# Performance work log

Hardware: AMD Instinct MI355X
Metric: run time of the kernel (lower is better)

## Reference

```python
import jax, jax.numpy as jnp
import numpy as np

B, T, C, H = 2, 2048, 1024, 16
D = C // H  # head_dim = 64

def setup_inputs() -> dict:
    key = jax.random.key(0)
    ks = jax.random.split(key, 5)
    x = jax.random.normal(ks[0], (B, T, C), dtype=jnp.float32)
    Wqkv = jax.random.normal(ks[1], (C, 3 * C), dtype=jnp.float32) * 0.02
    bqkv = jnp.zeros((3 * C,), dtype=jnp.float32)
    Wout = jax.random.normal(ks[2], (C, C), dtype=jnp.float32) * 0.02
    bout = jnp.zeros((C,), dtype=jnp.float32)
    return {"x": x, "Wqkv": Wqkv, "bqkv": bqkv, "Wout": Wout, "bout": bout}

def reference(x, Wqkv, bqkv, Wout, bout):
    Bb, Tt, Cc = x.shape
    qkv = x @ Wqkv + bqkv                       # [B,T,3C]
    qkv = qkv.reshape(Bb, Tt, 3, H, D)
    qkv = jnp.transpose(qkv, (2, 0, 3, 1, 4))   # [3,B,H,T,D]
    q, k, v = qkv[0], qkv[1], qkv[2]
    scale = 1.0 / np.sqrt(D).astype(np.float32)
    scores = jnp.einsum('bhqd,bhkd->bhqk', q, k) * scale  # [B,H,T,T]
    causal = jnp.tril(jnp.ones((Tt, Tt), dtype=bool))
    scores = jnp.where(causal[None, None, :, :], scores, jnp.float32(-jnp.inf))
    attn = jax.nn.softmax(scores, axis=-1)
    out = jnp.einsum('bhqk,bhkd->bhqd', attn, v)          # [B,H,T,D]
    out = jnp.transpose(out, (0, 2, 1, 3)).reshape(Bb, Tt, Cc)
    return out @ Wout + bout
```

## Files before the change

### kernel.cpp

```cpp
#include <hip/hip_runtime.h>

#define Bc 2
#define Tc 2048
#define Cc 1024
#define Hc 16
#define Dc 64
#define Mtot (Bc*Tc)
#define Kdim Cc
#define N1 (3*Cc)
#define N2 Cc

typedef __attribute__((ext_vector_type(8))) short short8;
typedef __attribute__((ext_vector_type(4))) float float4v;
typedef __attribute__((ext_vector_type(2))) unsigned int uint2v;
typedef __attribute__((ext_vector_type(4))) unsigned int uint4v;

#define HAVE_PLSWAP (__has_builtin(__builtin_amdgcn_permlane32_swap) && __has_builtin(__builtin_amdgcn_permlane16_swap))

__device__ __forceinline__ unsigned short f2bf(float f) {
  unsigned int u = __builtin_bit_cast(unsigned int, f);
  u += 0x7FFFu + ((u >> 16) & 1u);
  return (unsigned short)(u >> 16);
}

__device__ __forceinline__ unsigned int pk_bf16(float a, float b) {
#if __has_builtin(__builtin_amdgcn_cvt_pk_bf16_f32)
  typedef __attribute__((ext_vector_type(2))) __bf16 bf16x2;
  bf16x2 v = __builtin_amdgcn_cvt_pk_bf16_f32(a, b);
  return __builtin_bit_cast(unsigned int, v);
#else
  return (unsigned int)f2bf(a) | ((unsigned int)f2bf(b) << 16);
#endif
}

__device__ __forceinline__ float fast_exp2(float x) {
#if __has_builtin(__builtin_amdgcn_exp2f)
  return __builtin_amdgcn_exp2f(x);
#else
  return exp2f(x);
#endif
}

__device__ __forceinline__ void gl2lds16(const unsigned short* g, unsigned short* l) {
  __builtin_amdgcn_global_load_lds((const __attribute__((address_space(1))) void*)g,
                                   (__attribute__((address_space(3))) void*)l, 16, 0, 0);
}

#if HAVE_PLSWAP
__device__ __forceinline__ short8 pv_frag(unsigned int a, unsigned int b,
                                          unsigned int c, unsigned int d) {
  uint2v r0 = __builtin_amdgcn_permlane32_swap(a, c, false, false);
  uint2v r1 = __builtin_amdgcn_permlane16_swap(r0[0], r0[1], false, false);
  uint2v r2 = __builtin_amdgcn_permlane32_swap(b, d, false, false);
  uint2v r3 = __builtin_amdgcn_permlane16_swap(r2[0], r2[1], false, false);
  uint4v w = {r1[0], r3[0], r1[1], r3[1]};
  return __builtin_bit_cast(short8, w);
}
#endif

__global__ __launch_bounds__(256) void k_prep(const float* __restrict__ wqkv,
                                              const float* __restrict__ wout,
                                              const float* __restrict__ x,
                                              unsigned short* __restrict__ wqkvT,
                                              unsigned short* __restrict__ woutT,
                                              unsigned short* __restrict__ xb) {
  const int bx = blockIdx.x;
  if (bx >= 128) {
    int idx = ((bx - 128) * 32 + blockIdx.y) * 256 + threadIdx.x;
    float4 v = ((const float4*)x)[idx];
    uint2 o;
    o.x = pk_bf16(v.x, v.y);
    o.y = pk_bf16(v.z, v.w);
    ((uint2*)xb)[idx] = o;
    return;
  }
  __shared__ float tile[32][33];
  const float* w;  unsigned short* wT;  int N, n0;
  if (bx < 96) { w = wqkv; wT = wqkvT; N = N1; n0 = bx * 32; }
  else         { w = wout; wT = woutT; N = N2; n0 = (bx - 96) * 32; }
  const int k0 = blockIdx.y * 32;
  int tx = threadIdx.x & 31, ty = threadIdx.x >> 5;
  for (int i = 0; i < 4; ++i)
    tile[ty + 8*i][tx] = w[(size_t)(k0 + ty + 8*i) * N + n0 + tx];
  __syncthreads();
  for (int i = 0; i < 4; ++i)
    wT[(size_t)(n0 + ty + 8*i) * Kdim + k0 + tx] = f2bf(tile[tx][ty + 8*i]);
}

#define STAGE64(Abase, Bbase, dst, kb)                                          \
  for (int h2 = 0; h2 < 2; ++h2) {                                              \
    unsigned short* sa = (dst) + h2*4096;                                       \
    unsigned short* sb = (dst) + 8192 + h2*4096;                                \
    gl2lds16((Abase) + (size_t)(m0+row0)*Kdim + (kb) + 32*h2 + ko0, sa + c0*8); \
    gl2lds16((Abase) + (size_t)(m0+row1)*Kdim + (kb) + 32*h2 + ko1, sa + c1*8); \
    gl2lds16((Bbase) + (size_t)(n0+row0)*Kdim + (kb) + 32*h2 + ko0, sb + c0*8); \
    gl2lds16((Bbase) + (size_t)(n0+row1)*Kdim + (kb) + 32*h2 + ko1, sb + c1*8); \
  }

__global__ __launch_bounds__(256) void k_gemm_qkv(const unsigned short* __restrict__ A,
                                                  const unsigned short* __restrict__ BT,
                                                  const float* __restrict__ bias,
                                                  unsigned short* __restrict__ qkv) {
  __shared__ alignas(16) unsigned short smem[32768];
  const int m0 = blockIdx.y * 128, n0 = blockIdx.x * 128;
  const int tid = threadIdx.x;
  const int w = tid >> 6, lane = tid & 63;
  const int ln = lane & 15, qd = lane >> 4;
  const int wm = w >> 1, wn = w & 1;
  const int c0 = tid, c1 = tid + 256;
  const int row0 = c0 >> 2, ko0 = (c0 & 3) * 8;
  const int row1 = c1 >> 2, ko1 = (c1 & 3) * 8;
  const float4v zero4 = {0.f, 0.f, 0.f, 0.f};
  float4v acc[4][4];
  for (int i = 0; i < 4; ++i) for (int j = 0; j < 4; ++j) acc[i][j] = zero4;

  STAGE64(A, BT, smem, 0);
  int cur = 0;
  for (int kk = 0; kk < Kdim; kk += 64) {
    __syncthreads();
    if (kk + 64 < Kdim) {
      unsigned short* nb = smem + (cur ^ 1) * 16384;
      STAGE64(A, BT, nb, kk + 64);
    }
    const unsigned short* buf = smem + cur * 16384;
    for (int h = 0; h < 2; ++h) {
      const unsigned short* As = buf + h*4096;
      const unsigned short* Bs = buf + 8192 + h*4096;
      short8 af[4], bf[4];
      for (int i = 0; i < 4; ++i)
        af[i] = *(const short8*)(As + (wm*64 + i*16 + ln) * 32 + qd*8);
      for (int j = 0; j < 4; ++j)
        bf[j] = *(const short8*)(Bs + (wn*64 + j*16 + ln) * 32 + qd*8);
      for (int i = 0; i < 4; ++i)
        for (int j = 0; j < 4; ++j)
          acc[i][j] = __builtin_amdgcn_mfma_f32_16x16x32_bf16(af[i], bf[j], acc[i][j], 0, 0, 0);
    }
    cur ^= 1;
  }
  const int s = n0 >> 10;
  if (s < 2) {
    const float scale = (s == 0) ? 0.18033688f : 1.0f;
    for (int i = 0; i < 4; ++i) {
      int mbase = m0 + wm*64 + i*16 + qd*4;
      for (int j = 0; j < 4; ++j) {
        int ncol = n0 + wn*64 + j*16 + ln;
        float bv = bias[ncol];
        int rem = ncol & 1023;
        int h = rem >> 6, d = rem & 63;
        for (int r = 0; r < 4; ++r) {
          int m = mbase + r;
          int b = m >> 11, t = m & 2047;
          float val = (acc[i][j][r] + bv) * scale;
          qkv[((((size_t)s*Bc + b)*Hc + h)*Tc + t)*Dc + d] = f2bf(val);
        }
      }
    }
  } else {
    unsigned short* vbase = qkv + (size_t)2*Bc*Hc*Tc*Dc;
    const int b = m0 >> 11, t0 = m0 & 2047;
    const int h0 = (n0 & 1023) >> 6;
    for (int p = 0; p < 2; ++p) {
      __syncthreads();
      if (wn == p) {
        for (int i = 0; i < 4; ++i) {
          int tl = wm*64 + i*16 + qd*4;
          for (int j = 0; j < 4; ++j) {
            int dl = j*16 + ln;
            float bv = bias[n0 + p*64 + dl];
            uint2 pk;
            pk.x = pk_bf16(acc[i][j][0] + bv, acc[i][j][1] + bv);
            pk.y = pk_bf16(acc[i][j][2] + bv, acc[i][j][3] + bv);
            *(uint2*)(smem + dl*136 + tl) = pk;
          }
        }
      }
      __syncthreads();
      for (int ii = 0; ii < 4; ++ii) {
        int idx = tid + 256*ii;
        int row = idx >> 4, c16 = idx & 15;
        int4 v = *(const int4*)(smem + row*136 + c16*8);
        *(int4*)(vbase + (((size_t)b*Hc + h0 + p)*Dc + row)*Tc + t0 + c16*8) = v;
      }
    }
  }
}

__global__ __launch_bounds__(256) void k_gemm_out(const unsigned short* __restrict__ A,
                                                  const unsigned short* __restrict__ BT,
                                                  const float* __restrict__ bias,
                                                  float* __restrict__ out) {
  __shared__ alignas(16) unsigned short smem[32768];
  const int lin = blockIdx.y * 8 + blockIdx.x;
  const int swz = (lin & 7) * 32 + (lin >> 3);
  const int m0 = (swz >> 3) * 128, n0 = (swz & 7) * 128;
  const int tid = threadIdx.x;
  const int w = tid >> 6, lane = tid & 63;
  const int ln = lane & 15, qd = lane >> 4;
  const int wm = w >> 1, wn = w & 1;
  const int c0 = tid, c1 = tid + 256;
  const int row0 = c0 >> 2, ko0 = (c0 & 3) * 8;
  const int row1 = c1 >> 2, ko1 = (c1 & 3) * 8;
  const float4v zero4 = {0.f, 0.f, 0.f, 0.f};
  float4v acc[4][4];
  for (int i = 0; i < 4; ++i) for (int j = 0; j < 4; ++j) acc[i][j] = zero4;

  STAGE64(A, BT, smem, 0);
  int cur = 0;
  for (int kk = 0; kk < Kdim; kk += 64) {
    __syncthreads();
    if (kk + 64 < Kdim) {
      unsigned short* nb = smem + (cur ^ 1) * 16384;
      STAGE64(A, BT, nb, kk + 64);
    }
    const unsigned short* buf = smem + cur * 16384;
    for (int h = 0; h < 2; ++h) {
      const unsigned short* As = buf + h*4096;
      const unsigned short* Bs = buf + 8192 + h*4096;
      short8 af[4], bf[4];
      for (int i = 0; i < 4; ++i)
        af[i] = *(const short8*)(As + (wm*64 + i*16 + ln) * 32 + qd*8);
      for (int j = 0; j < 4; ++j)
        bf[j] = *(const short8*)(Bs + (wn*64 + j*16 + ln) * 32 + qd*8);
      for (int i = 0; i < 4; ++i)
        for (int j = 0; j < 4; ++j)
          acc[i][j] = __builtin_amdgcn_mfma_f32_16x16x32_bf16(af[i], bf[j], acc[i][j], 0, 0, 0);
    }
    cur ^= 1;
  }
  for (int i = 0; i < 4; ++i) {
    int mbase = m0 + wm*64 + i*16 + qd*4;
    for (int j = 0; j < 4; ++j) {
      int ncol = n0 + wn*64 + j*16 + ln;
      float bv = bias[ncol];
      for (int r = 0; r < 4; ++r)
        out[(size_t)(mbase + r) * N2 + ncol] = acc[i][j][r] + bv;
    }
  }
}

__device__ __forceinline__ void attn_substep(
    const short8* kf, const short8* va,
    unsigned short* __restrict__ pw,
    const short8 qa0, const short8 qa1,
    float4v* o, float& l_part,
    int k0, int myq, bool mask, int ln, int qd)
{
  const float4v zero4 = {0.f, 0.f, 0.f, 0.f};
  float4v s[4];
  for (int ki = 0; ki < 4; ++ki) {
    float4v z = zero4;
    z = __builtin_amdgcn_mfma_f32_16x16x32_bf16(kf[2*ki],     qa0, z, 0, 0, 0);
    s[ki] = __builtin_amdgcn_mfma_f32_16x16x32_bf16(kf[2*ki+1], qa1, z, 0, 0, 0);
  }
  if (mask) {
    for (int ki = 0; ki < 4; ++ki) {
      int key = k0 + ki*16 + qd*4;
      for (int r = 0; r < 4; ++r)
        if (key + r > myq) s[ki][r] = -1e30f;
    }
  }
  float st = 0.f;
  unsigned int pkw[4][2];
  for (int ki = 0; ki < 4; ++ki) {
    float p0 = fast_exp2(s[ki][0]);
    float p1 = fast_exp2(s[ki][1]);
    float p2 = fast_exp2(s[ki][2]);
    float p3 = fast_exp2(s[ki][3]);
    st += (p0 + p1) + (p2 + p3);
    pkw[ki][0] = pk_bf16(p0, p1);
    pkw[ki][1] = pk_bf16(p2, p3);
  }
  l_part += st;
#if HAVE_PLSWAP
  short8 pb0 = pv_frag(pkw[0][0], pkw[0][1], pkw[1][0], pkw[1][1]);
  short8 pb1 = pv_frag(pkw[2][0], pkw[2][1], pkw[3][0], pkw[3][1]);
#else
  for (int ki = 0; ki < 4; ++ki) {
    uint2 pk2; pk2.x = pkw[ki][0]; pk2.y = pkw[ki][1];
    *(uint2*)(pw + ln*72 + ki*16 + qd*4) = pk2;
  }
  short8 pb0 = *(const short8*)(pw + ln*72 + qd*8);
  short8 pb1 = *(const short8*)(pw + ln*72 + 32 + qd*8);
#endif
  for (int dt = 0; dt < 4; ++dt) {
    o[dt] = __builtin_amdgcn_mfma_f32_16x16x32_bf16(va[2*dt],   pb0, o[dt], 0, 0, 0);
    o[dt] = __builtin_amdgcn_mfma_f32_16x16x32_bf16(va[2*dt+1], pb1, o[dt], 0, 0, 0);
  }
}

__global__ __launch_bounds__(256) void k_attn(const unsigned short* __restrict__ qb,
                                              const unsigned short* __restrict__ kb,
                                              const unsigned short* __restrict__ vT,
                                              unsigned short* __restrict__ ob) {
  __shared__ alignas(16) unsigned short Ks[2][64*64];
  __shared__ alignas(16) unsigned short Vt[2][64*64];
#if !HAVE_PLSWAP
  __shared__ alignas(16) unsigned short Ps[4][16*72];
#endif
  const int bh = blockIdx.x;
  const int qt = 31 - blockIdx.y;
  const int tid = threadIdx.x;
  const int w = tid >> 6, lane = tid & 63;
  const int ln = lane & 15, qd = lane >> 4;
  const size_t base = (size_t)bh * Tc * Dc;
  const int b = bh >> 4, h = bh & 15;
  const float4v zero4 = {0.f, 0.f, 0.f, 0.f};
#if HAVE_PLSWAP
  unsigned short* pw = nullptr;
#else
  unsigned short* pw = Ps[w];
#endif

  const int srow = tid >> 3;
  const int sc_swz = ((tid & 7) ^ (srow & 7)) * 8;
  const int cs0 = ((qd)     ^ (ln & 7)) * 8;
  const int cs1 = ((4 + qd) ^ (ln & 7)) * 8;

  const int myq = qt*64 + w*16 + ln;
  const unsigned short* qr = qb + base + (size_t)myq * Dc;
  short8 qa0 = *(const short8*)(qr + qd*8);
  short8 qa1 = *(const short8*)(qr + 32 + qd*8);
  float4v o[4];
  for (int dt = 0; dt < 4; ++dt) o[dt] = zero4;
  float l = 0.f;

  gl2lds16(kb + base + (size_t)srow * Dc + sc_swz,        Ks[0] + tid*8);
  gl2lds16(kb + base + (size_t)(srow + 32) * Dc + sc_swz, Ks[0] + (tid + 256)*8);
  gl2lds16(vT + base + (size_t)srow * Tc + sc_swz,        Vt[0] + tid*8);
  gl2lds16(vT + base + (size_t)(srow + 32) * Tc + sc_swz, Vt[0] + (tid + 256)*8);
  __syncthreads();

  for (int kt = 0; kt <= qt; ++kt) {
    const int cur = kt & 1;
    if (kt < qt) {
      const int k0n = (kt + 1) * 64;
      const int nxt = cur ^ 1;
      gl2lds16(kb + base + (size_t)(k0n + srow) * Dc + sc_swz,      Ks[nxt] + tid*8);
      gl2lds16(kb + base + (size_t)(k0n + srow + 32) * Dc + sc_swz, Ks[nxt] + (tid + 256)*8);
      gl2lds16(vT + base + (size_t)srow * Tc + k0n + sc_swz,        Vt[nxt] + tid*8);
      gl2lds16(vT + base + (size_t)(srow + 32) * Tc + k0n + sc_swz, Vt[nxt] + (tid + 256)*8);
    }
    short8 kf[8], va[8];
    for (int ki = 0; ki < 4; ++ki) {
      const unsigned short* kr = Ks[cur] + (ki*16 + ln)*64;
      kf[2*ki]   = *(const short8*)(kr + cs0);
      kf[2*ki+1] = *(const short8*)(kr + cs1);
    }
    for (int dt = 0; dt < 4; ++dt) {
      const unsigned short* vr = Vt[cur] + (dt*16 + ln)*64;
      va[2*dt]   = *(const short8*)(vr + cs0);
      va[2*dt+1] = *(const short8*)(vr + cs1);
    }
    __builtin_amdgcn_s_setprio(1);
    attn_substep(kf, va, pw, qa0, qa1, o, l, kt*64, myq, kt == qt, ln, qd);
    __builtin_amdgcn_s_setprio(0);
    if (kt < qt)
      __syncthreads();
  }
  l += __shfl_xor(l, 16); l += __shfl_xor(l, 32);
  float inv = 1.0f / l;
  for (int dt = 0; dt < 4; ++dt) {
    uint2 ov;
    ov.x = pk_bf16(o[dt][0] * inv, o[dt][1] * inv);
    ov.y = pk_bf16(o[dt][2] * inv, o[dt][3] * inv);
    *(uint2*)(ob + (size_t)(b*Tc + myq)*Cc + h*Dc + dt*16 + qd*4) = ov;
  }
}

extern "C" void kernel_launch(void* const* d_in, const int* in_sizes, int n_in,
                              void* d_out, int out_size, void* d_ws, size_t ws_size,
                              hipStream_t stream) {
  const float* x    = (const float*)d_in[0];
  const float* Wqkv = (const float*)d_in[1];
  const float* bqkv = (const float*)d_in[2];
  const float* Wout = (const float*)d_in[3];
  const float* bout = (const float*)d_in[4];
  float* out = (float*)d_out;

  char* ws = (char*)d_ws;
  unsigned short* xb    = (unsigned short*)ws;
  unsigned short* wqkvT = (unsigned short*)(ws + 8388608);
  unsigned short* woutT = (unsigned short*)(ws + 14680064);
  unsigned short* qkvb  = (unsigned short*)(ws + 16777216);

  k_prep<<<dim3(256, 32), 256, 0, stream>>>(Wqkv, Wout, x, wqkvT, woutT, xb);
  k_gemm_qkv<<<dim3(N1/128, Mtot/128), 256, 0, stream>>>(xb, wqkvT, bqkv, qkvb);
  k_attn<<<dim3(32, 32), 256, 0, stream>>>(qkvb, qkvb + (size_t)Bc*Hc*Tc*Dc,
                                           qkvb + (size_t)2*Bc*Hc*Tc*Dc, xb);
  k_gemm_out<<<dim3(N2/128, Mtot/128), 256, 0, stream>>>(xb, woutT, bout, out);
}
```

Measured before the change: 173.2 us.

## Software-pipeline attention loop: defer PV MFMA of previous tile behind next QK

Restructures the attention inner loop so the P·V matrix multiplies for the previous key tile are issued at the start of the next iteration, before that tile's QK scores and softmax exponentials. V fragments and packed P fragments are carried across iterations in registers, and a tail step finishes the last tile. The aim is to overlap MFMA work with the exp/pack VALU work and LDS reads within one wave. It costs extra live registers (8 short8 plus two P fragments), which may reduce occupancy.

Result: no change. 170.7 us (-1.4%).

```diff
diff --git a/kernel.cpp b/kernel.cpp
--- a/kernel.cpp
+++ b/kernel.cpp
@@ -238,56 +238,6 @@
   }
 }
 
-__device__ __forceinline__ void attn_substep(
-    const short8* kf, const short8* va,
-    unsigned short* __restrict__ pw,
-    const short8 qa0, const short8 qa1,
-    float4v* o, float& l_part,
-    int k0, int myq, bool mask, int ln, int qd)
-{
-  const float4v zero4 = {0.f, 0.f, 0.f, 0.f};
-  float4v s[4];
-  for (int ki = 0; ki < 4; ++ki) {
-    float4v z = zero4;
-    z = __builtin_amdgcn_mfma_f32_16x16x32_bf16(kf[2*ki],     qa0, z, 0, 0, 0);
-    s[ki] = __builtin_amdgcn_mfma_f32_16x16x32_bf16(kf[2*ki+1], qa1, z, 0, 0, 0);
-  }
-  if (mask) {
-    for (int ki = 0; ki < 4; ++ki) {
-      int key = k0 + ki*16 + qd*4;
-      for (int r = 0; r < 4; ++r)
-        if (key + r > myq) s[ki][r] = -1e30f;
-    }
-  }
-  float st = 0.f;
-  unsigned int pkw[4][2];
-  for (int ki = 0; ki < 4; ++ki) {
-    float p0 = fast_exp2(s[ki][0]);
-    float p1 = fast_exp2(s[ki][1]);
-    float p2 = fast_exp2(s[ki][2]);
-    float p3 = fast_exp2(s[ki][3]);
-    st += (p0 + p1) + (p2 + p3);
-    pkw[ki][0] = pk_bf16(p0, p1);
-    pkw[ki][1] = pk_bf16(p2, p3);
-  }
-  l_part += st;
-#if HAVE_PLSWAP
-  short8 pb0 = pv_frag(pkw[0][0], pkw[0][1], pkw[1][0], pkw[1][1]);
-  short8 pb1 = pv_frag(pkw[2][0], pkw[2][1], pkw[3][0], pkw[3][1]);
-#else
-  for (int ki = 0; ki < 4; ++ki) {
-    uint2 pk2; pk2.x = pkw[ki][0]; pk2.y = pkw[ki][1];
-    *(uint2*)(pw + ln*72 + ki*16 + qd*4) = pk2;
-  }
-  short8 pb0 = *(const short8*)(pw + ln*72 + qd*8);
-  short8 pb1 = *(const short8*)(pw + ln*72 + 32 + qd*8);
-#endif
-  for (int dt = 0; dt < 4; ++dt) {
-    o[dt] = __builtin_amdgcn_mfma_f32_16x16x32_bf16(va[2*dt],   pb0, o[dt], 0, 0, 0);
-    o[dt] = __builtin_amdgcn_mfma_f32_16x16x32_bf16(va[2*dt+1], pb1, o[dt], 0, 0, 0);
-  }
-}
-
 __global__ __launch_bounds__(256) void k_attn(const unsigned short* __restrict__ qb,
                                               const unsigned short* __restrict__ kb,
                                               const unsigned short* __restrict__ vT,
@@ -305,9 +255,7 @@
   const size_t base = (size_t)bh * Tc * Dc;
   const int b = bh >> 4, h = bh & 15;
   const float4v zero4 = {0.f, 0.f, 0.f, 0.f};
-#if HAVE_PLSWAP
-  unsigned short* pw = nullptr;
-#else
+#if !HAVE_PLSWAP
   unsigned short* pw = Ps[w];
 #endif
 
@@ -323,6 +271,8 @@
   float4v o[4];
   for (int dt = 0; dt < 4; ++dt) o[dt] = zero4;
   float l = 0.f;
+  short8 vprev[8];
+  short8 pbA, pbB;
 
   gl2lds16(kb + base + (size_t)srow * Dc + sc_swz,        Ks[0] + tid*8);
   gl2lds16(kb + base + (size_t)(srow + 32) * Dc + sc_swz, Ks[0] + (tid + 256)*8);
@@ -330,32 +280,79 @@
   gl2lds16(vT + base + (size_t)(srow + 32) * Tc + sc_swz, Vt[0] + (tid + 256)*8);
   __syncthreads();
 
-  for (int kt = 0; kt <= qt; ++kt) {
-    const int cur = kt & 1;
-    if (kt < qt) {
-      const int k0n = (kt + 1) * 64;
+  for (int s = 0; s <= qt; ++s) {
+    const int cur = s & 1;
+    if (s < qt) {
+      const int k0n = (s + 1) * 64;
       const int nxt = cur ^ 1;
       gl2lds16(kb + base + (size_t)(k0n + srow) * Dc + sc_swz,      Ks[nxt] + tid*8);
       gl2lds16(kb + base + (size_t)(k0n + srow + 32) * Dc + sc_swz, Ks[nxt] + (tid + 256)*8);
       gl2lds16(vT + base + (size_t)srow * Tc + k0n + sc_swz,        Vt[nxt] + tid*8);
       gl2lds16(vT + base + (size_t)(srow + 32) * Tc + k0n + sc_swz, Vt[nxt] + (tid + 256)*8);
     }
-    short8 kf[8], va[8];
-    for (int ki = 0; ki < 4; ++ki) {
-      const unsigned short* kr = Ks[cur] + (ki*16 + ln)*64;
-      kf[2*ki]   = *(const short8*)(kr + cs0);
-      kf[2*ki+1] = *(const short8*)(kr + cs1);
-    }
-    for (int dt = 0; dt < 4; ++dt) {
-      const unsigned short* vr = Vt[cur] + (dt*16 + ln)*64;
-      va[2*dt]   = *(const short8*)(vr + cs0);
-      va[2*dt+1] = *(const short8*)(vr + cs1);
-    }
     __builtin_amdgcn_s_setprio(1);
-    attn_substep(kf, va, pw, qa0, qa1, o, l, kt*64, myq, kt == qt, ln, qd);
+    if (s > 0) {
+      for (int dt = 0; dt < 4; ++dt) {
+        o[dt] = __builtin_amdgcn_mfma_f32_16x16x32_bf16(vprev[2*dt],   pbA, o[dt], 0, 0, 0);
+        o[dt] = __builtin_amdgcn_mfma_f32_16x16x32_bf16(vprev[2*dt+1], pbB, o[dt], 0, 0, 0);
+      }
+    }
+    {
+      short8 kf[8];
+      for (int ki = 0; ki < 4; ++ki) {
+        const unsigned short* kr = Ks[cur] + (ki*16 + ln)*64;
+        kf[2*ki]   = *(const short8*)(kr + cs0);
+        kf[2*ki+1] = *(const short8*)(kr + cs1);
+      }
+      float4v sc[4];
+      for (int ki = 0; ki < 4; ++ki) {
+        float4v z = zero4;
+        z = __builtin_amdgcn_mfma_f32_16x16x32_bf16(kf[2*ki],     qa0, z, 0, 0, 0);
+        sc[ki] = __builtin_amdgcn_mfma_f32_16x16x32_bf16(kf[2*ki+1], qa1, z, 0, 0, 0);
+      }
+      if (s == qt) {
+        for (int ki = 0; ki < 4; ++ki) {
+          int key = s*64 + ki*16 + qd*4;
+          for (int r = 0; r < 4; ++r)
+            if (key + r > myq) sc[ki][r] = -1e30f;
+        }
+      }
+      for (int dt = 0; dt < 4; ++dt) {
+        const unsigned short* vr = Vt[cur] + (dt*16 + ln)*64;
+        vprev[2*dt]   = *(const short8*)(vr + cs0);
+        vprev[2*dt+1] = *(const short8*)(vr + cs1);
+      }
+      float st = 0.f;
+      unsigned int pkw[4][2];
+      for (int ki = 0; ki < 4; ++ki) {
+        float p0 = fast_exp2(sc[ki][0]);
+        float p1 = fast_exp2(sc[ki][1]);
+        float p2 = fast_exp2(sc[ki][2]);
+        float p3 = fast_exp2(sc[ki][3]);
+        st += (p0 + p1) + (p2 + p3);
+        pkw[ki][0] = pk_bf16(p0, p1);
+        pkw[ki][1] = pk_bf16(p2, p3);
+      }
+      l += st;
+#if HAVE_PLSWAP
+      pbA = pv_frag(pkw[0][0], pkw[0][1], pkw[1][0], pkw[1][1]);
+      pbB = pv_frag(pkw[2][0], pkw[2][1], pkw[3][0], pkw[3][1]);
+#else
+      for (int ki = 0; ki < 4; ++ki) {
+        uint2 pk2; pk2.x = pkw[ki][0]; pk2.y = pkw[ki][1];
+        *(uint2*)(pw + ln*72 + ki*16 + qd*4) = pk2;
+      }
+      pbA = *(const short8*)(pw + ln*72 + qd*8);
+      pbB = *(const short8*)(pw + ln*72 + 32 + qd*8);
+#endif
+    }
     __builtin_amdgcn_s_setprio(0);
-    if (kt < qt)
+    if (s < qt)
       __syncthreads();
+  }
+  for (int dt = 0; dt < 4; ++dt) {
+    o[dt] = __builtin_amdgcn_mfma_f32_16x16x32_bf16(vprev[2*dt],   pbA, o[dt], 0, 0, 0);
+    o[dt] = __builtin_amdgcn_mfma_f32_16x16x32_bf16(vprev[2*dt+1], pbB, o[dt], 0, 0, 0);
   }
   l += __shfl_xor(l, 16); l += __shfl_xor(l, 32);
   float inv = 1.0f / l;
```
